# Performance work log

Measured on AMD Instinct MI355X. Metric: run time of the kernel, lower is better.

The kernel has to match this reference:

```python
import jax, jax.numpy as jnp
import numpy as np

B, T, E = 2, 2048, 1024
H = 16
D = E // H  # head_dim = 64


def setup_inputs() -> dict:
    key = jax.random.key(0)
    k1, k2, k3 = jax.random.split(key, 3)
    x = jax.random.normal(k1, (B, T, E), dtype=jnp.float32)
    w_qkv = jax.random.normal(k2, (3 * E, E), dtype=jnp.float32) * 0.02
    w_proj = jax.random.normal(k3, (E, E), dtype=jnp.float32) * 0.02
    return {"x": x, "w_qkv": w_qkv, "w_proj": w_proj}


def reference(x, w_qkv, w_proj):
    b, t, c = x.shape
    # qkv projection (torch Linear: x @ W^T), split into q,k,v
    qkv = jnp.einsum('btc,fc->btf', x, w_qkv)  # [B,T,3E]
    q, k, v = jnp.split(qkv, 3, axis=-1)
    # [B,T,E] -> [B,H,T,D]
    q = q.reshape(b, t, H, D).transpose(0, 2, 1, 3)
    k = k.reshape(b, t, H, D).transpose(0, 2, 1, 3)
    v = v.reshape(b, t, H, D).transpose(0, 2, 1, 3)
    scale = 1.0 / jnp.sqrt(jnp.float32(D))
    att = jnp.einsum('bhqd,bhkd->bhqk', q, k) * scale  # [B,H,T,T]
    causal = jnp.tril(jnp.ones((t, t), dtype=bool))
    att = jnp.where(causal[None, None], att, -jnp.inf)
    att = jax.nn.softmax(att, axis=-1)
    out = jnp.einsum('bhqk,bhkd->bhqd', att, v)  # [B,H,T,D]
    out = out.transpose(0, 2, 1, 3).reshape(b, t, c)  # [B,T,E]
    out = jnp.einsum('btc,oc->bto', out, w_proj)
    return out
```

## Files before the change

kernel.cpp:

```cpp
#include <hip/hip_runtime.h>
#include <stdint.h>
#include <stddef.h>

typedef __attribute__((ext_vector_type(8))) short s16x8;
typedef __attribute__((ext_vector_type(4))) short s16x4;
typedef __attribute__((ext_vector_type(4))) float f32x4;

#define B_  2
#define T_  2048
#define E_  1024
#define H_  16
#define E3_ 3072

__device__ __forceinline__ short f2bf(float f) {
  union { float f; uint32_t u; } v; v.f = f;
  uint32_t u = v.u;
  return (short)((u + 0x7FFFu + ((u >> 16) & 1u)) >> 16);
}

__device__ __forceinline__ uint32_t fbits(float f) {
  union { float f; uint32_t u; } v; v.f = f; return v.u;
}

__device__ __forceinline__ void gload_lds16(const short* g, short* l) {
  __builtin_amdgcn_global_load_lds(
      (__attribute__((address_space(1))) void*)(const_cast<short*>(g)),
      (__attribute__((address_space(3))) void*)(l), 16, 0, 0);
}

__global__ void castk_all(const float* __restrict__ x, const float* __restrict__ wqkv,
                          const float* __restrict__ wproj, short* __restrict__ xb,
                          short* __restrict__ wqkvb, short* __restrict__ wprojb) {
  const int bid = blockIdx.x;
  const float* in; short* out; int i; float sc = 1.0f;
  if (bid < 4096)      { in = x;     out = xb;     i = bid * 256 + threadIdx.x; }
  else if (bid < 7168) { in = wqkv;  out = wqkvb;  i = (bid - 4096) * 256 + threadIdx.x;
                         if (i < 262144) sc = 0.18033688011112042f; }
  else                 { in = wproj; out = wprojb; i = (bid - 7168) * 256 + threadIdx.x; }
  const float4 v = ((const float4*)in)[i];
  s16x4 o;
  o[0] = f2bf(v.x * sc); o[1] = f2bf(v.y * sc);
  o[2] = f2bf(v.z * sc); o[3] = f2bf(v.w * sc);
  ((s16x4*)out)[i] = o;
}

template <int MODE>
__global__ void gemm_nt_128(const short* __restrict__ A, const short* __restrict__ B,
                            void* __restrict__ Cv, short* __restrict__ vt,
                            int M, int N, int K) {
  __shared__ short As[128 * 32];
  __shared__ short Bs[128 * 32];
  const int tid  = threadIdx.x;
  const int lane = tid & 63;
  const int w    = tid >> 6;
  const int quad = lane >> 4;
  const int l16  = lane & 15;
  const int wm   = (w >> 1) * 64;
  const int wn   = (w & 1) * 64;
  const int bm   = blockIdx.y * 128;
  const int bn   = blockIdx.x * 128;

  f32x4 acc[4][4];
#pragma unroll
  for (int i = 0; i < 4; i++)
#pragma unroll
    for (int j = 0; j < 4; j++) acc[i][j] = (f32x4){0.f, 0.f, 0.f, 0.f};

  const int srow = w * 32 + (lane >> 2);
  const int scol = (lane & 3) * 8;
  const short* gA = A + (size_t)(bm + srow) * K + scol;
  const short* gB = B + (size_t)(bn + srow) * K + scol;
  short* lA = As + (w * 32) * 32;
  short* lB = Bs + (w * 32) * 32;

  for (int k0 = 0; k0 < K; k0 += 32) {
    __syncthreads();
    gload_lds16(gA + k0,          lA);
    gload_lds16(gA + 16 * K + k0, lA + 16 * 32);
    gload_lds16(gB + k0,          lB);
    gload_lds16(gB + 16 * K + k0, lB + 16 * 32);
    __syncthreads();

    s16x8 a[4], b[4];
#pragma unroll
    for (int i = 0; i < 4; i++)
      a[i] = *(const s16x8*)&As[(wm + i * 16 + l16) * 32 + quad * 8];
#pragma unroll
    for (int j = 0; j < 4; j++)
      b[j] = *(const s16x8*)&Bs[(wn + j * 16 + l16) * 32 + quad * 8];
#pragma unroll
    for (int i = 0; i < 4; i++)
#pragma unroll
      for (int j = 0; j < 4; j++)
        acc[i][j] = __builtin_amdgcn_mfma_f32_16x16x32_bf16(a[i], b[j], acc[i][j], 0, 0, 0);
  }

  if (MODE == 2 && bn >= 2 * E_) {
#pragma unroll
    for (int i = 0; i < 4; i++) {
      const int token = bm + wm + i * 16 + quad * 4;
      const int bb = token >> 11, t = token & (T_ - 1);
#pragma unroll
      for (int j = 0; j < 4; j++) {
        const int col = bn + wn + j * 16 + l16 - 2 * E_;
        s16x4 pk;
#pragma unroll
        for (int r = 0; r < 4; r++) pk[r] = f2bf(acc[i][j][r]);
        *(s16x4*)&vt[((size_t)(bb * H_ + (col >> 6)) * 64 + (col & 63)) * T_ + t] = pk;
      }
    }
  } else {
#pragma unroll
    for (int i = 0; i < 4; i++) {
      const int row0 = bm + wm + i * 16 + quad * 4;
#pragma unroll
      for (int j = 0; j < 4; j++) {
        const int col = bn + wn + j * 16 + l16;
#pragma unroll
        for (int r = 0; r < 4; r++) {
          const size_t idx = (size_t)(row0 + r) * N + col;
          if (MODE == 2) ((short*)Cv)[idx] = f2bf(acc[i][j][r]);
          else           ((float*)Cv)[idx] = acc[i][j][r];
        }
      }
    }
  }
}

__global__ void __launch_bounds__(256, 2)
attn_kernel(const short* __restrict__ qkv, const short* __restrict__ vt,
            short* __restrict__ attout) {
  __shared__ short Ks[2][64 * 64];
  __shared__ short Vs[2][64 * 64];
  __shared__ short Ps[4][16 * 64];
  const int tid  = threadIdx.x;
  const int lane = tid & 63;
  const int w    = tid >> 6;
  const int quad = lane >> 4;
  const int l16  = lane & 15;
  const int bh = blockIdx.x;
  const int b = bh >> 4, h = bh & 15;
  const int pr = blockIdx.y;
  const float NEG_INF = -__builtin_inff();

  const int srl = lane >> 3;
  const int sgc = ((lane & 7) ^ srl) * 8;
  const short* gK = qkv + (size_t)(b * T_) * E3_ + E_ + h * 64 + sgc;
  const short* gV = vt + (size_t)(bh * 64) * T_ + sgc;
  const int swz = (l16 & 7);

  s16x8 ones;
#pragma unroll
  for (int i = 0; i < 8; i++) ones[i] = (short)0x3F80;

  auto stage = [&](int kv0s, int bf) {
#pragma unroll
    for (int i = 0; i < 2; i++) {
      const int row = w * 16 + i * 8 + srl;
      gload_lds16(gK + (size_t)(kv0s + row) * E3_, &Ks[bf][(w * 16 + i * 8) * 64]);
      gload_lds16(gV + (size_t)row * T_ + kv0s,    &Vs[bf][(w * 16 + i * 8) * 64]);
    }
  };

  stage(0, 0);
  __syncthreads();

  int g = 0;
#pragma unroll 1
  for (int ph = 0; ph < 2; ph++) {
    const int qt  = ph ? (31 - pr) : pr;
    const int q0b = qt * 64;
    const int q0w = q0b + w * 16;

    const short* qbase = qkv + (size_t)(b * T_ + q0w + l16) * E3_ + h * 64 + quad * 8;
    const s16x8 qf0 = *(const s16x8*)(qbase);
    const s16x8 qf1 = *(const s16x8*)(qbase + 32);

    f32x4 o[4]; f32x4 ol = (f32x4){0.f, 0.f, 0.f, 0.f};
#pragma unroll
    for (int j = 0; j < 4; j++) o[j] = (f32x4){0.f, 0.f, 0.f, 0.f};

    for (int kv0 = 0; kv0 <= q0b; kv0 += 64, g++) {
      const int cur = g & 1;

      s16x8 kf[2][4];
#pragma unroll
      for (int c = 0; c < 2; c++)
#pragma unroll
        for (int j = 0; j < 4; j++)
          kf[c][j] = *(const s16x8*)&Ks[cur][(j * 16 + l16) * 64 + (((c * 4 + quad) ^ swz) * 8)];

      if (kv0 + 64 <= q0b) stage(kv0 + 64, cur ^ 1);
      else if (ph == 0)    stage(0, cur ^ 1);

      f32x4 s[4];
#pragma unroll
      for (int j = 0; j < 4; j++) s[j] = (f32x4){0.f, 0.f, 0.f, 0.f};
#pragma unroll
      for (int c = 0; c < 2; c++)
#pragma unroll
        for (int j = 0; j < 4; j++)
          s[j] = __builtin_amdgcn_mfma_f32_16x16x32_bf16(kf[c][j], c == 0 ? qf0 : qf1, s[j], 0, 0, 0);

      if (kv0 == q0b) {
#pragma unroll
        for (int j = 0; j < 4; j++)
#pragma unroll
          for (int r = 0; r < 4; r++)
            if (j * 16 + quad * 4 + r > w * 16 + l16) s[j][r] = NEG_INF;
      }

#pragma unroll
      for (int j = 0; j < 4; j++) {
        const float p0 = exp2f(s[j][0]);
        const float p1 = exp2f(s[j][1]);
        const float p2 = exp2f(s[j][2]);
        const float p3 = exp2f(s[j][3]);
        int2 pk;
        pk.x = (int)__builtin_amdgcn_perm(fbits(p1), fbits(p0), 0x07060302u);
        pk.y = (int)__builtin_amdgcn_perm(fbits(p3), fbits(p2), 0x07060302u);
        short* pw = &Ps[w][l16 * 64 + (((2 * j + (quad >> 1)) ^ swz) * 8) + (quad & 1) * 4];
        *(int2*)pw = pk;
      }
      __asm volatile("s_waitcnt lgkmcnt(0)" ::: "memory");

#pragma unroll
      for (int c = 0; c < 2; c++) {
        const s16x8 pf = *(const s16x8*)&Ps[w][l16 * 64 + (((4 * c + quad) ^ swz) * 8)];
        ol = __builtin_amdgcn_mfma_f32_16x16x32_bf16(pf, ones, ol, 0, 0, 0);
#pragma unroll
        for (int j = 0; j < 4; j++) {
          const s16x8 vf = *(const s16x8*)&Vs[cur][(j * 16 + l16) * 64 + (((c * 4 + quad) ^ swz) * 8)];
          o[j] = __builtin_amdgcn_mfma_f32_16x16x32_bf16(pf, vf, o[j], 0, 0, 0);
        }
      }

      __syncthreads();
    }

#pragma unroll
    for (int r = 0; r < 4; r++) {
      const float inv = 1.0f / ol[r];
      const int q = q0w + quad * 4 + r;
      short* ob = attout + ((size_t)(b * T_ + q) * H_ + h) * 64 + l16;
      ob[0]  = f2bf(o[0][r] * inv);
      ob[16] = f2bf(o[1][r] * inv);
      ob[32] = f2bf(o[2][r] * inv);
      ob[48] = f2bf(o[3][r] * inv);
    }
  }
}

extern "C" void kernel_launch(void* const* d_in, const int* in_sizes, int n_in,
                              void* d_out, int out_size, void* d_ws, size_t ws_size,
                              hipStream_t stream) {
  const float* x     = (const float*)d_in[0];
  const float* wqkv  = (const float*)d_in[1];
  const float* wproj = (const float*)d_in[2];

  if (ws_size < 58720256u) return;
  short* ws     = (short*)d_ws;
  short* xb     = ws;
  short* wqkvb  = xb + 4194304;
  short* wprojb = wqkvb + 3145728;
  short* qkv    = wprojb + 1048576;
  short* vt     = qkv + 12582912;
  short* attb   = vt + 4194304;

  castk_all<<<8192, 256, 0, stream>>>(x, wqkv, wproj, xb, wqkvb, wprojb);
  gemm_nt_128<2><<<dim3(24, 32), 256, 0, stream>>>(xb, wqkvb, qkv, vt, 4096, 3072, 1024);
  attn_kernel<<<dim3(32, 16), 256, 0, stream>>>(qkv, vt, attb);
  gemm_nt_128<0><<<dim3(8, 32), 256, 0, stream>>>(attb, wprojb, d_out, nullptr, 4096, 1024, 1024);
}
```

Measured before the change: 174.8 us.

## Restructure attention to 2-wave blocks with 32 query rows per wave

Attention blocks shrink from 4 waves handling a pair of q-tiles (pr and 31-pr) to 2 waves each handling 32 query rows over a single q-tile. The grid grows to 32x32 and uses a snake ordering to balance the causal workload. Each wave reuses its K/V fragment loads across two 16-row subtiles, and MFMA sections are wrapped in s_setprio. The block count doubles and the pairing of short and long tiles is lost, so load balance now depends on the hardware scheduler. Register pressure per wave also rises.

```diff
diff --git a/kernel.cpp b/kernel.cpp
--- a/kernel.cpp
+++ b/kernel.cpp
@@ -127,12 +127,12 @@
   }
 }
 
-__global__ void __launch_bounds__(256, 2)
+__global__ void __launch_bounds__(128, 2)
 attn_kernel(const short* __restrict__ qkv, const short* __restrict__ vt,
             short* __restrict__ attout) {
   __shared__ short Ks[2][64 * 64];
   __shared__ short Vs[2][64 * 64];
-  __shared__ short Ps[4][16 * 64];
+  __shared__ short Ps[2][32 * 64];
   const int tid  = threadIdx.x;
   const int lane = tid & 63;
   const int w    = tid >> 6;
@@ -140,7 +140,9 @@
   const int l16  = lane & 15;
   const int bh = blockIdx.x;
   const int b = bh >> 4, h = bh & 15;
-  const int pr = blockIdx.y;
+  const int ya = blockIdx.y & 7, yb = blockIdx.y >> 3;
+  const int qt = yb * 8 + ((yb & 1) ? (7 - ya) : ya);
+  const int q0b = qt * 64;
   const float NEG_INF = -__builtin_inff();
 
   const int srl = lane >> 3;
@@ -155,100 +157,117 @@
 
   auto stage = [&](int kv0s, int bf) {
 #pragma unroll
-    for (int i = 0; i < 2; i++) {
-      const int row = w * 16 + i * 8 + srl;
-      gload_lds16(gK + (size_t)(kv0s + row) * E3_, &Ks[bf][(w * 16 + i * 8) * 64]);
-      gload_lds16(gV + (size_t)row * T_ + kv0s,    &Vs[bf][(w * 16 + i * 8) * 64]);
+    for (int i = 0; i < 4; i++) {
+      const int row = w * 32 + i * 8 + srl;
+      gload_lds16(gK + (size_t)(kv0s + row) * E3_, &Ks[bf][(w * 32 + i * 8) * 64]);
+      gload_lds16(gV + (size_t)row * T_ + kv0s,    &Vs[bf][(w * 32 + i * 8) * 64]);
     }
   };
+
+  s16x8 qf[2][2];
+#pragma unroll
+  for (int sub = 0; sub < 2; sub++) {
+    const short* qbase = qkv + (size_t)(b * T_ + q0b + w * 32 + sub * 16 + l16) * E3_ + h * 64 + quad * 8;
+    qf[sub][0] = *(const s16x8*)(qbase);
+    qf[sub][1] = *(const s16x8*)(qbase + 32);
+  }
+
+  f32x4 o[2][4], ol[2];
+#pragma unroll
+  for (int sub = 0; sub < 2; sub++) {
+    ol[sub] = (f32x4){0.f, 0.f, 0.f, 0.f};
+#pragma unroll
+    for (int j = 0; j < 4; j++) o[sub][j] = (f32x4){0.f, 0.f, 0.f, 0.f};
+  }
 
   stage(0, 0);
   __syncthreads();
 
-  int g = 0;
-#pragma unroll 1
-  for (int ph = 0; ph < 2; ph++) {
-    const int qt  = ph ? (31 - pr) : pr;
-    const int q0b = qt * 64;
-    const int q0w = q0b + w * 16;
-
-    const short* qbase = qkv + (size_t)(b * T_ + q0w + l16) * E3_ + h * 64 + quad * 8;
-    const s16x8 qf0 = *(const s16x8*)(qbase);
-    const s16x8 qf1 = *(const s16x8*)(qbase + 32);
-
-    f32x4 o[4]; f32x4 ol = (f32x4){0.f, 0.f, 0.f, 0.f};
-#pragma unroll
-    for (int j = 0; j < 4; j++) o[j] = (f32x4){0.f, 0.f, 0.f, 0.f};
-
-    for (int kv0 = 0; kv0 <= q0b; kv0 += 64, g++) {
-      const int cur = g & 1;
-
-      s16x8 kf[2][4];
-#pragma unroll
-      for (int c = 0; c < 2; c++)
+  for (int kv0 = 0, g = 0; kv0 <= q0b; kv0 += 64, g++) {
+    const int cur = g & 1;
+
+    if (kv0 + 64 <= q0b) stage(kv0 + 64, cur ^ 1);
+
+    f32x4 s[2][4];
+#pragma unroll
+    for (int sub = 0; sub < 2; sub++)
+#pragma unroll
+      for (int j = 0; j < 4; j++) s[sub][j] = (f32x4){0.f, 0.f, 0.f, 0.f};
+
+    __builtin_amdgcn_s_setprio(1);
+#pragma unroll
+    for (int c = 0; c < 2; c++) {
+      s16x8 kf[4];
+#pragma unroll
+      for (int j = 0; j < 4; j++)
+        kf[j] = *(const s16x8*)&Ks[cur][(j * 16 + l16) * 64 + (((c * 4 + quad) ^ swz) * 8)];
+#pragma unroll
+      for (int sub = 0; sub < 2; sub++)
 #pragma unroll
         for (int j = 0; j < 4; j++)
-          kf[c][j] = *(const s16x8*)&Ks[cur][(j * 16 + l16) * 64 + (((c * 4 + quad) ^ swz) * 8)];
-
-      if (kv0 + 64 <= q0b) stage(kv0 + 64, cur ^ 1);
-      else if (ph == 0)    stage(0, cur ^ 1);
-
-      f32x4 s[4];
-#pragma unroll
-      for (int j = 0; j < 4; j++) s[j] = (f32x4){0.f, 0.f, 0.f, 0.f};
-#pragma unroll
-      for (int c = 0; c < 2; c++)
+          s[sub][j] = __builtin_amdgcn_mfma_f32_16x16x32_bf16(kf[j], qf[sub][c], s[sub][j], 0, 0, 0);
+    }
+    __builtin_amdgcn_s_setprio(0);
+
+    if (kv0 == q0b) {
+#pragma unroll
+      for (int sub = 0; sub < 2; sub++)
 #pragma unroll
         for (int j = 0; j < 4; j++)
-          s[j] = __builtin_amdgcn_mfma_f32_16x16x32_bf16(kf[c][j], c == 0 ? qf0 : qf1, s[j], 0, 0, 0);
-
-      if (kv0 == q0b) {
-#pragma unroll
-        for (int j = 0; j < 4; j++)
 #pragma unroll
           for (int r = 0; r < 4; r++)
-            if (j * 16 + quad * 4 + r > w * 16 + l16) s[j][r] = NEG_INF;
-      }
-
+            if (j * 16 + quad * 4 + r > w * 32 + sub * 16 + l16) s[sub][j][r] = NEG_INF;
+    }
+
+#pragma unroll
+    for (int sub = 0; sub < 2; sub++)
 #pragma unroll
       for (int j = 0; j < 4; j++) {
-        const float p0 = exp2f(s[j][0]);
-        const float p1 = exp2f(s[j][1]);
-        const float p2 = exp2f(s[j][2]);
-        const float p3 = exp2f(s[j][3]);
+        const float p0 = exp2f(s[sub][j][0]);
+        const float p1 = exp2f(s[sub][j][1]);
+        const float p2 = exp2f(s[sub][j][2]);
+        const float p3 = exp2f(s[sub][j][3]);
         int2 pk;
         pk.x = (int)__builtin_amdgcn_perm(fbits(p1), fbits(p0), 0x07060302u);
         pk.y = (int)__builtin_amdgcn_perm(fbits(p3), fbits(p2), 0x07060302u);
-        short* pw = &Ps[w][l16 * 64 + (((2 * j + (quad >> 1)) ^ swz) * 8) + (quad & 1) * 4];
+        short* pw = &Ps[w][(sub * 16 + l16) * 64 + (((2 * j + (quad >> 1)) ^ swz) * 8) + (quad & 1) * 4];
         *(int2*)pw = pk;
       }
-      __asm volatile("s_waitcnt lgkmcnt(0)" ::: "memory");
-
-#pragma unroll
-      for (int c = 0; c < 2; c++) {
-        const s16x8 pf = *(const s16x8*)&Ps[w][l16 * 64 + (((4 * c + quad) ^ swz) * 8)];
-        ol = __builtin_amdgcn_mfma_f32_16x16x32_bf16(pf, ones, ol, 0, 0, 0);
-#pragma unroll
-        for (int j = 0; j < 4; j++) {
-          const s16x8 vf = *(const s16x8*)&Vs[cur][(j * 16 + l16) * 64 + (((c * 4 + quad) ^ swz) * 8)];
-          o[j] = __builtin_amdgcn_mfma_f32_16x16x32_bf16(pf, vf, o[j], 0, 0, 0);
-        }
-      }
-
-      __syncthreads();
-    }
-
+    __asm volatile("s_waitcnt lgkmcnt(0)" ::: "memory");
+
+    __builtin_amdgcn_s_setprio(1);
+#pragma unroll
+    for (int c = 0; c < 2; c++) {
+      s16x8 vf[4];
+#pragma unroll
+      for (int j = 0; j < 4; j++)
+        vf[j] = *(const s16x8*)&Vs[cur][(j * 16 + l16) * 64 + (((c * 4 + quad) ^ swz) * 8)];
+#pragma unroll
+      for (int sub = 0; sub < 2; sub++) {
+        const s16x8 pf = *(const s16x8*)&Ps[w][(sub * 16 + l16) * 64 + (((4 * c + quad) ^ swz) * 8)];
+        ol[sub] = __builtin_amdgcn_mfma_f32_16x16x32_bf16(pf, ones, ol[sub], 0, 0, 0);
+#pragma unroll
+        for (int j = 0; j < 4; j++)
+          o[sub][j] = __builtin_amdgcn_mfma_f32_16x16x32_bf16(pf, vf[j], o[sub][j], 0, 0, 0);
+      }
+    }
+    __builtin_amdgcn_s_setprio(0);
+
+    __syncthreads();
+  }
+
+#pragma unroll
+  for (int sub = 0; sub < 2; sub++)
 #pragma unroll
     for (int r = 0; r < 4; r++) {
-      const float inv = 1.0f / ol[r];
-      const int q = q0w + quad * 4 + r;
+      const float inv = 1.0f / ol[sub][r];
+      const int q = q0b + w * 32 + sub * 16 + quad * 4 + r;
       short* ob = attout + ((size_t)(b * T_ + q) * H_ + h) * 64 + l16;
-      ob[0]  = f2bf(o[0][r] * inv);
-      ob[16] = f2bf(o[1][r] * inv);
-      ob[32] = f2bf(o[2][r] * inv);
-      ob[48] = f2bf(o[3][r] * inv);
-    }
-  }
+      ob[0]  = f2bf(o[sub][0][r] * inv);
+      ob[16] = f2bf(o[sub][1][r] * inv);
+      ob[32] = f2bf(o[sub][2][r] * inv);
+      ob[48] = f2bf(o[sub][3][r] * inv);
+    }
 }
 
 extern "C" void kernel_launch(void* const* d_in, const int* in_sizes, int n_in,
@@ -269,6 +288,6 @@
 
   castk_all<<<8192, 256, 0, stream>>>(x, wqkv, wproj, xb, wqkvb, wprojb);
   gemm_nt_128<2><<<dim3(24, 32), 256, 0, stream>>>(xb, wqkvb, qkv, vt, 4096, 3072, 1024);
-  attn_kernel<<<dim3(32, 16), 256, 0, stream>>>(qkv, vt, attb);
+  attn_kernel<<<dim3(32, 32), 128, 0, stream>>>(qkv, vt, attb);
   gemm_nt_128<0><<<dim3(8, 32), 256, 0, stream>>>(attb, wprojb, d_out, nullptr, 4096, 1024, 1024);
 }
```

Measured after the change: 189.6 us. 1.08x slower.
